# Kernel tuning notes

Hardware: AMD Instinct MI355X
Metric: run time of the kernel (lower is better)

## Reference

```python
import jax, jax.numpy as jnp
import numpy as np

N = 200000
D = 64
NNZ = 6400000
NUM_LAYERS = 4
CURVE = 1.0
MIN_NORM = 1e-15
EPS = 1e-7  # float32 clamp eps for arcosh domain


def logmap0_hyperboloid(x, c):
    # Lorentz-model log map at the origin (HGCN Hyperboloid.logmap0).
    # x: [N, D] points on hyperboloid; first coord is the time component.
    K = 1.0 / c
    sqrtK = K ** 0.5
    y = x[:, 1:]                                             # [N, D-1]
    y_norm = jnp.maximum(
        jnp.linalg.norm(y, axis=-1, keepdims=True), MIN_NORM)
    theta = jnp.maximum(x[:, 0:1] / sqrtK, 1.0 + EPS)
    res = sqrtK * jnp.arccosh(theta) * y / y_norm            # [N, D-1]
    return jnp.concatenate([jnp.zeros_like(x[:, :1]), res], axis=-1)


def spmm(rows, cols, vals, x):
    # COO sparse [N,N] @ dense [N,D]
    return jax.ops.segment_sum(vals[:, None] * x[cols], rows, num_segments=N)


def setup_inputs() -> dict:
    key = jax.random.key(0)
    k1, k2, k3, k4 = jax.random.split(key, 4)
    # Build valid hyperboloid points: x0 = sqrt(K + ||y||^2)
    y = jax.random.normal(k1, (N, D - 1), dtype=jnp.float32)
    K = 1.0 / CURVE
    x0 = jnp.sqrt(K + jnp.sum(y * y, axis=-1, keepdims=True))
    x = jnp.concatenate([x0, y], axis=-1)                    # [N, D]
    rows = jax.random.randint(k2, (NNZ,), 0, N, dtype=jnp.int32)
    cols = jax.random.randint(k3, (NNZ,), 0, N, dtype=jnp.int32)
    vals = jax.random.uniform(k4, (NNZ,), dtype=jnp.float32) / 32.0
    return {"x": x, "rows": rows, "cols": cols, "vals": vals}


def reference(x, rows, cols, vals):
    h = logmap0_hyperboloid(x, CURVE)
    # denseGCN: output[0]=h; output[i+1] = sum(output[1:i+1]) + A @ output[i]
    # Maintain running sum S = sum(output[1:i+1]) instead of re-summing (O(L) not O(L^2)).
    prev = h          # output[i]
    S = jnp.zeros_like(h)
    for i in range(NUM_LAYERS):
        cur = S + spmm(rows, cols, vals, prev) if i > 0 else spmm(rows, cols, vals, prev)
        S = S + cur
        prev = cur
    return prev
```

## Files before the change

### kernel.cpp

```cpp
#include <hip/hip_runtime.h>
#include <hip/hip_fp16.h>

#define SCAN_T 256
#define DELTA 512
#define LOG_DELTA 9
#define CAP 20480
#define PA_CHUNK 8192
#define MAXB 512
#define NPH 32
#define PHSHIFT 13

typedef unsigned long long u64;

__global__ void compute_h_kernel(const float* __restrict__ x, __half2* __restrict__ h, int N) {
    int hw = (blockIdx.x * blockDim.x + threadIdx.x) >> 5;
    if (hw >= N) return;
    int l = threadIdx.x & 31;
    const float2* x2 = (const float2*)x;
    float2 v = x2[hw * 32 + l];
    float y2 = (l == 0) ? v.y * v.y : v.x * v.x + v.y * v.y;
    #pragma unroll
    for (int m = 16; m >= 1; m >>= 1) y2 += __shfl_xor(y2, m, 32);
    float x0 = __shfl(v.x, 0, 32);
    float ynorm = fmaxf(sqrtf(y2), 1e-15f);
    float theta = fmaxf(x0, 1.0f + 1e-7f);
    float alpha = acoshf(theta) / ynorm;
    float2 r = (l == 0) ? make_float2(0.0f, v.y * alpha)
                        : make_float2(v.x * alpha, v.y * alpha);
    h[hw * 32 + l] = __float22half2_rn(r);
}

__device__ __forceinline__ int block_incl_scan(int x) {
    __shared__ int sh[SCAN_T];
    int t = threadIdx.x;
    sh[t] = x; __syncthreads();
    for (int ofs = 1; ofs < SCAN_T; ofs <<= 1) {
        int y = (t >= ofs) ? sh[t - ofs] : 0;
        __syncthreads();
        x += y; sh[t] = x;
        __syncthreads();
    }
    return x;
}

__global__ void pass_a_kernel(const int* __restrict__ rows, const int* __restrict__ cols,
                              const float* __restrict__ vals, int* __restrict__ fill,
                              u64* __restrict__ slab, int nnz, int NB) {
    __shared__ int cnt[MAXB];
    __shared__ int cur[MAXB];
    int t = threadIdx.x;
    int start = blockIdx.x * PA_CHUNK;
    int end = min(start + PA_CHUNK, nnz);
    for (int i = t; i < NB; i += 256) cnt[i] = 0;
    __syncthreads();
    for (int e = start + t; e < end; e += 256)
        atomicAdd(&cnt[rows[e] >> LOG_DELTA], 1);
    __syncthreads();
    for (int i = t; i < NB; i += 256) {
        int c = cnt[i];
        cur[i] = (c > 0) ? atomicAdd(&fill[i], c) : 0;
    }
    __syncthreads();
    for (int e = start + t; e < end; e += 256) {
        int r = rows[e];
        int bkt = r >> LOG_DELTA;
        int lr = r & (DELTA - 1);
        int pos = atomicAdd(&cur[bkt], 1);
        if (pos < CAP) {
            u64 hi = ((u64)(((unsigned)lr << 18) | (unsigned)cols[e])) << 32;
            slab[(size_t)bkt * CAP + pos] = hi | (u64)__float_as_uint(vals[e]);
        }
    }
}

__global__ void bucket_scan_kernel(const int* __restrict__ fill, int* __restrict__ csr_base,
                                   int* __restrict__ row_ptr, int NB, int N, int nnz) {
    int t = threadIdx.x;
    int a0 = (2 * t < NB) ? fill[2 * t] : 0;
    int a1 = (2 * t + 1 < NB) ? fill[2 * t + 1] : 0;
    int s = a0 + a1;
    int incl = block_incl_scan(s);
    int excl = incl - s;
    if (2 * t < NB) csr_base[2 * t] = excl;
    if (2 * t + 1 < NB) csr_base[2 * t + 1] = excl + a0;
    if (t == 0) row_ptr[N] = nnz;
}

__global__ void pass_b_kernel(const int* __restrict__ fill, const u64* __restrict__ slab,
                              const int* __restrict__ csr_base, u64* __restrict__ edges,
                              int* __restrict__ row_ptr, int N) {
    __shared__ int bins[DELTA * NPH];
    int b = blockIdx.x;
    int t = threadIdx.x;
    for (int i = t; i < DELTA * NPH; i += 256) bins[i] = 0;
    __syncthreads();
    int m = fill[b];
    if (m > CAP) m = CAP;
    const u64* sl = slab + (size_t)b * CAP;
    for (int e = t; e < m; e += 256) {
        u64 u = sl[e];
        int lr = (int)(u >> 50);
        int col = (int)((u >> 32) & 0x3FFFFu);
        atomicAdd(&bins[lr * NPH + (col >> PHSHIFT)], 1);
    }
    __syncthreads();
    int base = t * 64;
    int s = 0;
    #pragma unroll 4
    for (int k = 0; k < 64; ++k) s += bins[base + k];
    int incl = block_incl_scan(s);
    int run = incl - s;
    for (int k = 0; k < 64; ++k) { int c = bins[base + k]; bins[base + k] = run; run += c; }
    __syncthreads();
    int cb = csr_base[b];
    int base_row = b * DELTA;
    for (int lr = t; lr < DELTA; lr += 256) {
        int row = base_row + lr;
        if (row < N) row_ptr[row] = cb + bins[lr * NPH];
    }
    __syncthreads();
    for (int e = t; e < m; e += 256) {
        u64 u = sl[e];
        int lr = (int)(u >> 50);
        unsigned col = (unsigned)(u >> 32) & 0x3FFFFu;
        unsigned vb = (unsigned)u;
        int pos = cb + atomicAdd(&bins[lr * NPH + (int)(col >> PHSHIFT)], 1);
        edges[pos] = ((u64)vb << 32) | col;
    }
}

__device__ __forceinline__ void spmm_row(const int* __restrict__ row_ptr,
                                         const u64* __restrict__ edges,
                                         const __half2* __restrict__ pin,
                                         int hw, int l, float& accx, float& accy) {
    int j = row_ptr[hw];
    int end = row_ptr[hw + 1];
    accx = 0.0f; accy = 0.0f;
    for (; j + 8 <= end; j += 8) {
        u64 e0 = __builtin_nontemporal_load(&edges[j]);
        u64 e1 = __builtin_nontemporal_load(&edges[j + 1]);
        u64 e2 = __builtin_nontemporal_load(&edges[j + 2]);
        u64 e3 = __builtin_nontemporal_load(&edges[j + 3]);
        u64 e4 = __builtin_nontemporal_load(&edges[j + 4]);
        u64 e5 = __builtin_nontemporal_load(&edges[j + 5]);
        u64 e6 = __builtin_nontemporal_load(&edges[j + 6]);
        u64 e7 = __builtin_nontemporal_load(&edges[j + 7]);
        float2 f0 = __half22float2(pin[(int)(e0 & 0xFFFFFFFFu) * 32 + l]);
        float2 f1 = __half22float2(pin[(int)(e1 & 0xFFFFFFFFu) * 32 + l]);
        float2 f2 = __half22float2(pin[(int)(e2 & 0xFFFFFFFFu) * 32 + l]);
        float2 f3 = __half22float2(pin[(int)(e3 & 0xFFFFFFFFu) * 32 + l]);
        float2 f4 = __half22float2(pin[(int)(e4 & 0xFFFFFFFFu) * 32 + l]);
        float2 f5 = __half22float2(pin[(int)(e5 & 0xFFFFFFFFu) * 32 + l]);
        float2 f6 = __half22float2(pin[(int)(e6 & 0xFFFFFFFFu) * 32 + l]);
        float2 f7 = __half22float2(pin[(int)(e7 & 0xFFFFFFFFu) * 32 + l]);
        float v0 = __int_as_float((int)(e0 >> 32)), v1 = __int_as_float((int)(e1 >> 32));
        float v2 = __int_as_float((int)(e2 >> 32)), v3 = __int_as_float((int)(e3 >> 32));
        float v4 = __int_as_float((int)(e4 >> 32)), v5 = __int_as_float((int)(e5 >> 32));
        float v6 = __int_as_float((int)(e6 >> 32)), v7 = __int_as_float((int)(e7 >> 32));
        accx = fmaf(v0, f0.x, accx); accy = fmaf(v0, f0.y, accy);
        accx = fmaf(v1, f1.x, accx); accy = fmaf(v1, f1.y, accy);
        accx = fmaf(v2, f2.x, accx); accy = fmaf(v2, f2.y, accy);
        accx = fmaf(v3, f3.x, accx); accy = fmaf(v3, f3.y, accy);
        accx = fmaf(v4, f4.x, accx); accy = fmaf(v4, f4.y, accy);
        accx = fmaf(v5, f5.x, accx); accy = fmaf(v5, f5.y, accy);
        accx = fmaf(v6, f6.x, accx); accy = fmaf(v6, f6.y, accy);
        accx = fmaf(v7, f7.x, accx); accy = fmaf(v7, f7.y, accy);
    }
    for (; j < end; ++j) {
        u64 e = __builtin_nontemporal_load(&edges[j]);
        float2 f = __half22float2(pin[(int)(e & 0xFFFFFFFFu) * 32 + l]);
        float v = __int_as_float((int)(e >> 32));
        accx = fmaf(v, f.x, accx); accy = fmaf(v, f.y, accy);
    }
}

__global__ void spmm_kernel(const int* __restrict__ row_ptr, const u64* __restrict__ edges,
                            const __half2* __restrict__ pin, __half2* __restrict__ pout, int N) {
    int hw = (blockIdx.x * blockDim.x + threadIdx.x) >> 5;
    if (hw >= N) return;
    int l = threadIdx.x & 31;
    float accx, accy;
    spmm_row(row_ptr, edges, pin, hw, l, accx, accy);
    pout[hw * 32 + l] = __float22half2_rn(make_float2(accx, accy));
}

__global__ void spmm_final_kernel(const int* __restrict__ row_ptr, const u64* __restrict__ edges,
                                  const __half2* __restrict__ p1, const __half2* __restrict__ p2,
                                  const __half2* __restrict__ p3, float2* __restrict__ out, int N) {
    int hw = (blockIdx.x * blockDim.x + threadIdx.x) >> 5;
    if (hw >= N) return;
    int l = threadIdx.x & 31;
    float accx, accy;
    spmm_row(row_ptr, edges, p3, hw, l, accx, accy);
    int idx = hw * 32 + l;
    float2 f1 = __half22float2(p1[idx]);
    float2 f2 = __half22float2(p2[idx]);
    float2 f3 = __half22float2(p3[idx]);
    float ox = fmaf(4.0f, f1.x, fmaf(5.0f, f2.x, fmaf(3.0f, f3.x, accx)));
    float oy = fmaf(4.0f, f1.y, fmaf(5.0f, f2.y, fmaf(3.0f, f3.y, accy)));
    out[idx] = make_float2(ox, oy);
}

extern "C" void kernel_launch(void* const* d_in, const int* in_sizes, int n_in,
                              void* d_out, int out_size, void* d_ws, size_t ws_size,
                              hipStream_t stream) {
    const float* x    = (const float*)d_in[0];
    const int*   rows = (const int*)d_in[1];
    const int*   cols = (const int*)d_in[2];
    const float* vals = (const float*)d_in[3];
    float2* out = (float2*)d_out;
    const int D = 64;
    const int N = in_sizes[0] / D;
    const int nnz = in_sizes[1];
    const int NB = (N + DELTA - 1) / DELTA;

    char* ws = (char*)d_ws;
    size_t off = 0;
    auto alloc = [&](size_t bytes) -> void* {
        void* p = ws + off;
        off = (off + bytes + 255) & ~(size_t)255;
        return p;
    };
    int*     fill     = (int*)alloc((size_t)MAXB * 4);
    int*     csr_base = (int*)alloc((size_t)MAXB * 4);
    int*     row_ptr  = (int*)alloc((size_t)(N + 1) * 4);
    u64*     slab     = (u64*)alloc((size_t)NB * CAP * 8);
    u64*     edges    = (u64*)alloc((size_t)nnz * 8);
    __half2* B0 = (__half2*)alloc((size_t)N * D * 2);
    __half2* B1 = (__half2*)alloc((size_t)N * D * 2);
    __half2* B2 = (__half2*)alloc((size_t)N * D * 2);
    (void)ws_size; (void)n_in; (void)out_size;

    hipMemsetAsync(fill, 0, (size_t)MAXB * 4, stream);

    const int rblocks = (N + 7) / 8;
    compute_h_kernel<<<rblocks, 256, 0, stream>>>(x, B0, N);

    int pa_blocks = (nnz + PA_CHUNK - 1) / PA_CHUNK;
    pass_a_kernel<<<pa_blocks, 256, 0, stream>>>(rows, cols, vals, fill, slab, nnz, NB);
    bucket_scan_kernel<<<1, 256, 0, stream>>>(fill, csr_base, row_ptr, NB, N, nnz);
    pass_b_kernel<<<NB, 256, 0, stream>>>(fill, slab, csr_base, edges, row_ptr, N);

    spmm_kernel<<<rblocks, 256, 0, stream>>>(row_ptr, edges, B0, B1, N);
    spmm_kernel<<<rblocks, 256, 0, stream>>>(row_ptr, edges, B1, B2, N);
    spmm_kernel<<<rblocks, 256, 0, stream>>>(row_ptr, edges, B2, B0, N);
    spmm_final_kernel<<<rblocks, 256, 0, stream>>>(row_ptr, edges, B1, B2, B0, out, N);
}
```

Measured before the change: 1.019 ms.

## Sweep column phases across blocks so concurrent rows gather from a shared column window

Pass B now stores a per-row, per-column-phase pointer table alongside row_ptr. Each SpMM block takes a global ticket from an atomic clock and maps it to a column phase, so every row starts at that phase's edges and wraps around. Blocks running at the same time then gather from a similar slice of the input feature matrix, aiming for better L2/MALL reuse of the random gathers. In exchange it writes and reads a large extra pointer array (N*32 ints), adds an atomic plus a block barrier per block, and shrinks the unroll from 8 to 4 with two loop segments per row.

```diff
diff --git a/kernel.cpp b/kernel.cpp
--- a/kernel.cpp
+++ b/kernel.cpp
@@ -8,6 +8,7 @@
 #define PA_CHUNK 8192
 #define MAXB 512
 #define NPH 32
+#define NPH_USED 25
 #define PHSHIFT 13
 
 typedef unsigned long long u64;
@@ -88,7 +89,7 @@
 
 __global__ void pass_b_kernel(const int* __restrict__ fill, const u64* __restrict__ slab,
                               const int* __restrict__ csr_base, u64* __restrict__ edges,
-                              int* __restrict__ row_ptr, int N) {
+                              int* __restrict__ row_ptr, int* __restrict__ pptr, int N) {
     __shared__ int bins[DELTA * NPH];
     int b = blockIdx.x;
     int t = threadIdx.x;
@@ -118,6 +119,10 @@
         int row = base_row + lr;
         if (row < N) row_ptr[row] = cb + bins[lr * NPH];
     }
+    for (int i = t; i < DELTA * NPH; i += 256) {
+        int row = base_row + (i >> 5);
+        if (row < N) pptr[(size_t)base_row * NPH + i] = cb + bins[i];
+    }
     __syncthreads();
     for (int e = t; e < m; e += 256) {
         u64 u = sl[e];
@@ -129,42 +134,25 @@
     }
 }
 
-__device__ __forceinline__ void spmm_row(const int* __restrict__ row_ptr,
-                                         const u64* __restrict__ edges,
+__device__ __forceinline__ void spmm_seg(const u64* __restrict__ edges,
                                          const __half2* __restrict__ pin,
-                                         int hw, int l, float& accx, float& accy) {
-    int j = row_ptr[hw];
-    int end = row_ptr[hw + 1];
-    accx = 0.0f; accy = 0.0f;
-    for (; j + 8 <= end; j += 8) {
+                                         int l, int j, int end,
+                                         float& accx, float& accy) {
+    for (; j + 4 <= end; j += 4) {
         u64 e0 = __builtin_nontemporal_load(&edges[j]);
         u64 e1 = __builtin_nontemporal_load(&edges[j + 1]);
         u64 e2 = __builtin_nontemporal_load(&edges[j + 2]);
         u64 e3 = __builtin_nontemporal_load(&edges[j + 3]);
-        u64 e4 = __builtin_nontemporal_load(&edges[j + 4]);
-        u64 e5 = __builtin_nontemporal_load(&edges[j + 5]);
-        u64 e6 = __builtin_nontemporal_load(&edges[j + 6]);
-        u64 e7 = __builtin_nontemporal_load(&edges[j + 7]);
         float2 f0 = __half22float2(pin[(int)(e0 & 0xFFFFFFFFu) * 32 + l]);
         float2 f1 = __half22float2(pin[(int)(e1 & 0xFFFFFFFFu) * 32 + l]);
         float2 f2 = __half22float2(pin[(int)(e2 & 0xFFFFFFFFu) * 32 + l]);
         float2 f3 = __half22float2(pin[(int)(e3 & 0xFFFFFFFFu) * 32 + l]);
-        float2 f4 = __half22float2(pin[(int)(e4 & 0xFFFFFFFFu) * 32 + l]);
-        float2 f5 = __half22float2(pin[(int)(e5 & 0xFFFFFFFFu) * 32 + l]);
-        float2 f6 = __half22float2(pin[(int)(e6 & 0xFFFFFFFFu) * 32 + l]);
-        float2 f7 = __half22float2(pin[(int)(e7 & 0xFFFFFFFFu) * 32 + l]);
         float v0 = __int_as_float((int)(e0 >> 32)), v1 = __int_as_float((int)(e1 >> 32));
         float v2 = __int_as_float((int)(e2 >> 32)), v3 = __int_as_float((int)(e3 >> 32));
-        float v4 = __int_as_float((int)(e4 >> 32)), v5 = __int_as_float((int)(e5 >> 32));
-        float v6 = __int_as_float((int)(e6 >> 32)), v7 = __int_as_float((int)(e7 >> 32));
         accx = fmaf(v0, f0.x, accx); accy = fmaf(v0, f0.y, accy);
         accx = fmaf(v1, f1.x, accx); accy = fmaf(v1, f1.y, accy);
         accx = fmaf(v2, f2.x, accx); accy = fmaf(v2, f2.y, accy);
         accx = fmaf(v3, f3.x, accx); accy = fmaf(v3, f3.y, accy);
-        accx = fmaf(v4, f4.x, accx); accy = fmaf(v4, f4.y, accy);
-        accx = fmaf(v5, f5.x, accx); accy = fmaf(v5, f5.y, accy);
-        accx = fmaf(v6, f6.x, accx); accy = fmaf(v6, f6.y, accy);
-        accx = fmaf(v7, f7.x, accx); accy = fmaf(v7, f7.y, accy);
     }
     for (; j < end; ++j) {
         u64 e = __builtin_nontemporal_load(&edges[j]);
@@ -174,24 +162,47 @@
     }
 }
 
-__global__ void spmm_kernel(const int* __restrict__ row_ptr, const u64* __restrict__ edges,
-                            const __half2* __restrict__ pin, __half2* __restrict__ pout, int N) {
+__device__ __forceinline__ int sweep_phase(unsigned* clk, int nb) {
+    __shared__ int sph;
+    if (threadIdx.x == 0) {
+        unsigned g = atomicAdd(clk, 1u);
+        sph = (int)(((g % (unsigned)nb) * (unsigned)NPH_USED) / (unsigned)nb);
+    }
+    __syncthreads();
+    return sph;
+}
+
+__global__ void spmm_kernel(const int* __restrict__ row_ptr, const int* __restrict__ pptr,
+                            const u64* __restrict__ edges, const __half2* __restrict__ pin,
+                            __half2* __restrict__ pout, int N, int nb, unsigned* clk) {
+    int sph = sweep_phase(clk, nb);
     int hw = (blockIdx.x * blockDim.x + threadIdx.x) >> 5;
     if (hw >= N) return;
     int l = threadIdx.x & 31;
-    float accx, accy;
-    spmm_row(row_ptr, edges, pin, hw, l, accx, accy);
+    int start = row_ptr[hw];
+    int end = row_ptr[hw + 1];
+    int j0 = pptr[(size_t)hw * NPH + sph];
+    float accx = 0.0f, accy = 0.0f;
+    spmm_seg(edges, pin, l, j0, end, accx, accy);
+    spmm_seg(edges, pin, l, start, j0, accx, accy);
     pout[hw * 32 + l] = __float22half2_rn(make_float2(accx, accy));
 }
 
-__global__ void spmm_final_kernel(const int* __restrict__ row_ptr, const u64* __restrict__ edges,
+__global__ void spmm_final_kernel(const int* __restrict__ row_ptr, const int* __restrict__ pptr,
+                                  const u64* __restrict__ edges,
                                   const __half2* __restrict__ p1, const __half2* __restrict__ p2,
-                                  const __half2* __restrict__ p3, float2* __restrict__ out, int N) {
+                                  const __half2* __restrict__ p3, float2* __restrict__ out,
+                                  int N, int nb, unsigned* clk) {
+    int sph = sweep_phase(clk, nb);
     int hw = (blockIdx.x * blockDim.x + threadIdx.x) >> 5;
     if (hw >= N) return;
     int l = threadIdx.x & 31;
-    float accx, accy;
-    spmm_row(row_ptr, edges, p3, hw, l, accx, accy);
+    int start = row_ptr[hw];
+    int end = row_ptr[hw + 1];
+    int j0 = pptr[(size_t)hw * NPH + sph];
+    float accx = 0.0f, accy = 0.0f;
+    spmm_seg(edges, p3, l, j0, end, accx, accy);
+    spmm_seg(edges, p3, l, start, j0, accx, accy);
     int idx = hw * 32 + l;
     float2 f1 = __half22float2(p1[idx]);
     float2 f2 = __half22float2(p2[idx]);
@@ -221,17 +232,20 @@
         off = (off + bytes + 255) & ~(size_t)255;
         return p;
     };
-    int*     fill     = (int*)alloc((size_t)MAXB * 4);
-    int*     csr_base = (int*)alloc((size_t)MAXB * 4);
-    int*     row_ptr  = (int*)alloc((size_t)(N + 1) * 4);
-    u64*     slab     = (u64*)alloc((size_t)NB * CAP * 8);
-    u64*     edges    = (u64*)alloc((size_t)nnz * 8);
-    __half2* B0 = (__half2*)alloc((size_t)N * D * 2);
-    __half2* B1 = (__half2*)alloc((size_t)N * D * 2);
-    __half2* B2 = (__half2*)alloc((size_t)N * D * 2);
+    int*      fill     = (int*)alloc((size_t)MAXB * 4);
+    int*      csr_base = (int*)alloc((size_t)MAXB * 4);
+    unsigned* clk      = (unsigned*)alloc(256);
+    int*      row_ptr  = (int*)alloc((size_t)(N + 1) * 4);
+    int*      pptr     = (int*)alloc((size_t)NB * DELTA * NPH * 4);
+    u64*      slab     = (u64*)alloc((size_t)NB * CAP * 8);
+    u64*      edges    = (u64*)alloc((size_t)nnz * 8);
+    __half2*  B0 = (__half2*)alloc((size_t)N * D * 2);
+    __half2*  B1 = (__half2*)alloc((size_t)N * D * 2);
+    __half2*  B2 = (__half2*)alloc((size_t)N * D * 2);
     (void)ws_size; (void)n_in; (void)out_size;
 
     hipMemsetAsync(fill, 0, (size_t)MAXB * 4, stream);
+    hipMemsetAsync(clk, 0, 4, stream);
 
     const int rblocks = (N + 7) / 8;
     compute_h_kernel<<<rblocks, 256, 0, stream>>>(x, B0, N);
@@ -239,10 +253,10 @@
     int pa_blocks = (nnz + PA_CHUNK - 1) / PA_CHUNK;
     pass_a_kernel<<<pa_blocks, 256, 0, stream>>>(rows, cols, vals, fill, slab, nnz, NB);
     bucket_scan_kernel<<<1, 256, 0, stream>>>(fill, csr_base, row_ptr, NB, N, nnz);
-    pass_b_kernel<<<NB, 256, 0, stream>>>(fill, slab, csr_base, edges, row_ptr, N);
-
-    spmm_kernel<<<rblocks, 256, 0, stream>>>(row_ptr, edges, B0, B1, N);
-    spmm_kernel<<<rblocks, 256, 0, stream>>>(row_ptr, edges, B1, B2, N);
-    spmm_kernel<<<rblocks, 256, 0, stream>>>(row_ptr, edges, B2, B0, N);
-    spmm_final_kernel<<<rblocks, 256, 0, stream>>>(row_ptr, edges, B1, B2, B0, out, N);
-}
+    pass_b_kernel<<<NB, 256, 0, stream>>>(fill, slab, csr_base, edges, row_ptr, pptr, N);
+
+    spmm_kernel<<<rblocks, 256, 0, stream>>>(row_ptr, pptr, edges, B0, B1, N, rblocks, clk);
+    spmm_kernel<<<rblocks, 256, 0, stream>>>(row_ptr, pptr, edges, B1, B2, N, rblocks, clk);
+    spmm_kernel<<<rblocks, 256, 0, stream>>>(row_ptr, pptr, edges, B2, B0, N, rblocks, clk);
+    spmm_final_kernel<<<rblocks, 256, 0, stream>>>(row_ptr, pptr, edges, B1, B2, B0, out, N, rblocks, clk);
+}
```

After: 1.737 ms. 70.4% more time.
